# Kernel optimization log

Hardware: AMD Instinct MI355X
Metric: run time of the kernel (lower is better)

The kernel has to match this reference:

```python
import jax, jax.numpy as jnp
import numpy as np

V, D, M, R = 100000, 256, 8192, 32
B_SZ, L = 2048, 100


def setup_inputs() -> dict:
    key = jax.random.key(0)
    k1, k2, k3, k4 = jax.random.split(key, 4)
    ids = jax.random.randint(k1, (B_SZ, L), 0, V, dtype=jnp.int64)
    idx = jnp.arange(M, dtype=jnp.int64)  # unique adapter row ids
    E = jax.random.normal(k2, (V, D), dtype=jnp.float32)
    A_rows = jax.random.normal(k3, (M, R), dtype=jnp.float32) * (1.0 / np.sqrt(R))
    Bm = jax.random.normal(k4, (D, R), dtype=jnp.float32) * (1.0 / np.sqrt(R))
    return {"ids": ids, "idx": idx, "E": E, "A_rows": A_rows, "B": Bm}


def reference(ids, idx, E, A_rows, B):
    # base embedding gather: [B, L, D]
    base = E[ids]
    # Equivalent to the one-hot matmul (idx unique): map each vocab id to its
    # adapter-row position, -1 if not adapted.
    pos = jnp.full((V,), -1, dtype=jnp.int32).at[idx].set(
        jnp.arange(idx.shape[0], dtype=jnp.int32))
    p = pos[ids]                      # [B, L]
    hit = (p >= 0)[..., None]         # [B, L, 1]
    A_sel = jnp.where(hit, A_rows[jnp.clip(p, 0)], 0.0)  # [B, L, R]
    delta = jnp.einsum('blr,dr->bld', A_sel, B)           # [B, L, D]
    return base + delta
```

## Files before the change

kernel.cpp:

```cpp
#include <hip/hip_runtime.h>

#define V_SZ   100000
#define D_SZ   256
#define M_SZ   8192
#define R_SZ   32
#define NTOK   (2048 * 100)


__global__ void init_pos_kernel(int* __restrict__ pos, int n) {
    int i = blockIdx.x * blockDim.x + threadIdx.x;
    if (i < n) pos[i] = -1;
}

__global__ void scatter_pos_kernel(const int* __restrict__ idx, int* __restrict__ pos, int m) {
    int i = blockIdx.x * blockDim.x + threadIdx.x;
    if (i < m) pos[idx[i]] = i;
}

__global__ void transpose_b_kernel(const float* __restrict__ Bm, float* __restrict__ Bt) {
    int i = blockIdx.x * blockDim.x + threadIdx.x;
    if (i < D_SZ * R_SZ) {
        int d = i >> 5;
        int r = i & (R_SZ - 1);
        Bt[r * D_SZ + d] = Bm[i];
    }
}


__global__ __launch_bounds__(256) void fuse_kernel(
    const int*   __restrict__ ids,
    const float* __restrict__ E,
    const float* __restrict__ A_rows,
    const float* __restrict__ Bt,
    const int*   __restrict__ pos,
    float*       __restrict__ out) {

    const int lane = threadIdx.x & 63;
    const int wave = (int)((blockIdx.x * blockDim.x + threadIdx.x) >> 6);
    const int nw   = (int)((gridDim.x * blockDim.x) >> 6);
    const int dofs = lane * 4;

    for (int tk = wave; tk < NTOK; tk += nw) {
        const int id = ids[tk];
        const int p  = pos[id];

        const float4 e = *(const float4*)(E + (size_t)id * D_SZ + dofs);
        float4 o = e;

        if (p >= 0) {
            const int ps = __builtin_amdgcn_readfirstlane(p);
            const float* __restrict__ Ar = A_rows + (size_t)ps * R_SZ;
            float ax = 0.f, ay = 0.f, az = 0.f, aw = 0.f;
            #pragma unroll 4
            for (int r = 0; r < R_SZ; ++r) {
                const float a  = Ar[r];
                const float4 b = *(const float4*)(Bt + r * D_SZ + dofs);
                ax += a * b.x; ay += a * b.y; az += a * b.z; aw += a * b.w;
            }
            o.x += ax; o.y += ay; o.z += az; o.w += aw;
        }

        *(float4*)(out + (size_t)tk * D_SZ + dofs) = o;
    }
}


extern "C" void kernel_launch(void* const* d_in, const int* in_sizes, int n_in,
                              void* d_out, int out_size, void* d_ws, size_t ws_size,
                              hipStream_t stream) {
    const int*   ids    = (const int*)  d_in[0];
    const int*   idx    = (const int*)  d_in[1];
    const float* E      = (const float*)d_in[2];
    const float* A_rows = (const float*)d_in[3];
    const float* Bm     = (const float*)d_in[4];
    float*       out    = (float*)      d_out;

    int*   pos = (int*)d_ws;
    size_t pos_bytes = ((size_t)V_SZ * sizeof(int) + 255) & ~(size_t)255;
    float* Bt  = (float*)((char*)d_ws + pos_bytes);

    {
        int threads = 256;
        int blocks  = (V_SZ + threads - 1) / threads;
        hipLaunchKernelGGL(init_pos_kernel, dim3(blocks), dim3(threads), 0, stream, pos, V_SZ);
    }
    {
        int threads = 256;
        int blocks  = (M_SZ + threads - 1) / threads;
        hipLaunchKernelGGL(scatter_pos_kernel, dim3(blocks), dim3(threads), 0, stream, idx, pos, M_SZ);
    }
    {
        int threads = 256;
        int blocks  = (D_SZ * R_SZ + threads - 1) / threads;
        hipLaunchKernelGGL(transpose_b_kernel, dim3(blocks), dim3(threads), 0, stream, Bm, Bt);
    }
    {
        hipLaunchKernelGGL(fuse_kernel, dim3(4096), dim3(256), 0, stream,
                           ids, E, A_rows, Bt, pos, out);
    }
}
```

Measured before the change: 338.7 us.

## Batch token gathers per wave, merge setup kernels, use nontemporal output stores

Each wave now handles a fixed block of 16 tokens. It loads their ids and adapter positions in a single coalesced read and broadcasts them by shuffle. It then issues 8 embedding-row gathers before any compute, so more loads are in flight to hide gather latency. The scatter and transpose setup kernels are merged into one launch, position init is vectorized, and output writes use nontemporal stores so they do not pollute the cache. The gather arrays raise register pressure, and the grid is now sized exactly to the token count.

```diff
diff --git a/kernel.cpp b/kernel.cpp
--- a/kernel.cpp
+++ b/kernel.cpp
@@ -5,20 +5,22 @@
 #define M_SZ   8192
 #define R_SZ   32
 #define NTOK   (2048 * 100)
+#define TPW    16
+#define BATCH  8
+
+typedef float f4_t __attribute__((ext_vector_type(4)));
 
 
-__global__ void init_pos_kernel(int* __restrict__ pos, int n) {
+__global__ __launch_bounds__(256) void init_pos_kernel(int4* __restrict__ pos4) {
     int i = blockIdx.x * blockDim.x + threadIdx.x;
-    if (i < n) pos[i] = -1;
+    if (i < V_SZ / 4) pos4[i] = make_int4(-1, -1, -1, -1);
 }
 
-__global__ void scatter_pos_kernel(const int* __restrict__ idx, int* __restrict__ pos, int m) {
+__global__ __launch_bounds__(256) void scatter_and_transpose_kernel(
+    const int* __restrict__ idx, int* __restrict__ pos,
+    const float* __restrict__ Bm, float* __restrict__ Bt) {
     int i = blockIdx.x * blockDim.x + threadIdx.x;
-    if (i < m) pos[idx[i]] = i;
-}
-
-__global__ void transpose_b_kernel(const float* __restrict__ Bm, float* __restrict__ Bt) {
-    int i = blockIdx.x * blockDim.x + threadIdx.x;
+    if (i < M_SZ) pos[idx[i]] = i;
     if (i < D_SZ * R_SZ) {
         int d = i >> 5;
         int r = i & (R_SZ - 1);
@@ -36,31 +38,46 @@
     float*       __restrict__ out) {
 
     const int lane = threadIdx.x & 63;
-    const int wave = (int)((blockIdx.x * blockDim.x + threadIdx.x) >> 6);
-    const int nw   = (int)((gridDim.x * blockDim.x) >> 6);
+    const int wv   = (int)(blockIdx.x * (blockDim.x >> 6) + (threadIdx.x >> 6));
+    const int base = wv * TPW;
     const int dofs = lane * 4;
 
-    for (int tk = wave; tk < NTOK; tk += nw) {
-        const int id = ids[tk];
-        const int p  = pos[id];
+    int myid = 0, myp = -1;
+    if (lane < TPW) {
+        myid = ids[base + lane];
+        myp  = pos[myid];
+    }
 
-        const float4 e = *(const float4*)(E + (size_t)id * D_SZ + dofs);
-        float4 o = e;
+    #pragma unroll
+    for (int t0 = 0; t0 < TPW; t0 += BATCH) {
+        float4 e[BATCH];
+        int    pv[BATCH];
 
-        if (p >= 0) {
-            const int ps = __builtin_amdgcn_readfirstlane(p);
-            const float* __restrict__ Ar = A_rows + (size_t)ps * R_SZ;
-            float ax = 0.f, ay = 0.f, az = 0.f, aw = 0.f;
-            #pragma unroll 4
-            for (int r = 0; r < R_SZ; ++r) {
-                const float a  = Ar[r];
-                const float4 b = *(const float4*)(Bt + r * D_SZ + dofs);
-                ax += a * b.x; ay += a * b.y; az += a * b.z; aw += a * b.w;
-            }
-            o.x += ax; o.y += ay; o.z += az; o.w += aw;
+        #pragma unroll
+        for (int j = 0; j < BATCH; ++j) {
+            const int id = __shfl(myid, t0 + j);
+            pv[j]        = __shfl(myp,  t0 + j);
+            e[j] = *(const float4*)(E + (size_t)id * D_SZ + dofs);
         }
 
-        *(float4*)(out + (size_t)tk * D_SZ + dofs) = o;
+        #pragma unroll
+        for (int j = 0; j < BATCH; ++j) {
+            float4 o = e[j];
+            const int ps = __builtin_amdgcn_readfirstlane(pv[j]);
+            if (ps >= 0) {
+                const float* __restrict__ Ar = A_rows + (size_t)ps * R_SZ;
+                float ax = 0.f, ay = 0.f, az = 0.f, aw = 0.f;
+                #pragma unroll 8
+                for (int r = 0; r < R_SZ; ++r) {
+                    const float a  = Ar[r];
+                    const float4 b = *(const float4*)(Bt + r * D_SZ + dofs);
+                    ax += a * b.x; ay += a * b.y; az += a * b.z; aw += a * b.w;
+                }
+                o.x += ax; o.y += ay; o.z += az; o.w += aw;
+            }
+            f4_t v = { o.x, o.y, o.z, o.w };
+            __builtin_nontemporal_store(v, (f4_t*)(out + (size_t)(base + t0 + j) * D_SZ + dofs));
+        }
     }
 }
 
@@ -80,22 +97,17 @@
     float* Bt  = (float*)((char*)d_ws + pos_bytes);
 
     {
-        int threads = 256;
-        int blocks  = (V_SZ + threads - 1) / threads;
-        hipLaunchKernelGGL(init_pos_kernel, dim3(blocks), dim3(threads), 0, stream, pos, V_SZ);
+        int n = V_SZ / 4;
+        hipLaunchKernelGGL(init_pos_kernel, dim3((n + 255) / 256), dim3(256), 0, stream,
+                           (int4*)pos);
     }
     {
-        int threads = 256;
-        int blocks  = (M_SZ + threads - 1) / threads;
-        hipLaunchKernelGGL(scatter_pos_kernel, dim3(blocks), dim3(threads), 0, stream, idx, pos, M_SZ);
+        int n = (M_SZ > D_SZ * R_SZ) ? M_SZ : D_SZ * R_SZ;
+        hipLaunchKernelGGL(scatter_and_transpose_kernel, dim3((n + 255) / 256), dim3(256),
+                           0, stream, idx, pos, Bm, Bt);
     }
     {
-        int threads = 256;
-        int blocks  = (D_SZ * R_SZ + threads - 1) / threads;
-        hipLaunchKernelGGL(transpose_b_kernel, dim3(blocks), dim3(threads), 0, stream, Bm, Bt);
-    }
-    {
-        hipLaunchKernelGGL(fuse_kernel, dim3(4096), dim3(256), 0, stream,
+        hipLaunchKernelGGL(fuse_kernel, dim3(NTOK / (TPW * 4)), dim3(256), 0, stream,
                            ids, E, A_rows, Bt, pos, out);
     }
 }
```

Result: faster. 327.6 us (-3.3%).
